# Performance work log

Measured on AMD Instinct MI355X. Metric: run time of the kernel, lower is better.

Reference implementation:

```python
import jax, jax.numpy as jnp
import numpy as np

D_MODEL = 1024
H = 16
D_K = D_MODEL // H


def setup_inputs() -> dict:
    key = jax.random.key(0)
    ks = jax.random.split(key, 8)
    B, S = 2, 2048
    q = jax.random.normal(ks[0], (B, S, D_MODEL), dtype=jnp.float32)
    k = jax.random.normal(ks[1], (B, S, D_MODEL), dtype=jnp.float32)
    v = jax.random.normal(ks[2], (B, S, D_MODEL), dtype=jnp.float32)
    mask = jnp.ones((B, 1, S), dtype=jnp.int32)  # key-padding mask, 1 = keep
    sc = 1.0 / np.sqrt(D_MODEL)
    # torch Linear weights [out, in]
    Wq = jax.random.normal(ks[3], (D_MODEL, D_MODEL), dtype=jnp.float32) * sc
    Wk = jax.random.normal(ks[4], (D_MODEL, D_MODEL), dtype=jnp.float32) * sc
    Wv = jax.random.normal(ks[5], (D_MODEL, D_MODEL), dtype=jnp.float32) * sc
    Wo = jax.random.normal(ks[6], (D_MODEL, D_MODEL), dtype=jnp.float32) * sc
    return {"q": q, "k": k, "v": v, "mask": mask,
            "Wq": Wq, "Wk": Wk, "Wv": Wv, "Wo": Wo}


def reference(q, k, v, mask, Wq, Wk, Wv, Wo):
    B, Sq, _ = q.shape
    Sk = k.shape[1]
    # projections (torch Linear: x @ W.T), split heads -> [B, H, S, d_k]
    def split_heads(x, W, S):
        return (x @ W.T).reshape(B, S, H, D_K).transpose(0, 2, 1, 3)
    qh = split_heads(q, Wq, Sq)
    kh = split_heads(k, Wk, Sk)
    vh = split_heads(v, Wv, Sk)
    scores = jnp.einsum('bhqd,bhkd->bhqk', qh, kh) / jnp.sqrt(
        jnp.asarray(D_K, qh.dtype))
    # mask.unsqueeze(1): [B,1,S] -> [B,1,1,S]; masked_fill(mask==0, -1e9)
    m = mask[:, None, :, :]
    scores = jnp.where(m == 0, jnp.asarray(-1e9, scores.dtype), scores)
    p = jax.nn.softmax(scores, axis=-1)
    out = jnp.einsum('bhqk,bhkd->bhqd', p, vh)
    out = out.transpose(0, 2, 1, 3).reshape(B, Sq, H * D_K)
    return out @ Wo.T
```

## Files before the change

### kernel.cpp

```cpp
#include <hip/hip_runtime.h>
#include <hip/hip_bf16.h>

#define LOG2E 1.4426950408889634f

typedef __attribute__((ext_vector_type(8))) __bf16 bf16x8;
typedef __attribute__((ext_vector_type(2))) __bf16 bf16x2;
typedef __attribute__((ext_vector_type(4))) float f32x4;
typedef __attribute__((ext_vector_type(16))) float f32x16;

#define MFMA16(a,b,c) __builtin_amdgcn_mfma_f32_16x16x32_bf16((a),(b),(c),0,0,0)
#define MFMA32(a,b,c) __builtin_amdgcn_mfma_f32_32x32x16_bf16((a),(b),(c),0,0,0)

#define GLL16(g, l) __builtin_amdgcn_global_load_lds( \
    (const __attribute__((address_space(1))) void*)(g), \
    (__attribute__((address_space(3))) void*)(l), 16, 0, 0)

__device__ __forceinline__ unsigned short bfu(float f) {
    __bf16 h = (__bf16)f; unsigned short u; __builtin_memcpy(&u, &h, 2); return u;
}
__device__ __forceinline__ unsigned cvtpk(float lo, float hi) {
    bf16x2 t; t.x = (__bf16)lo; t.y = (__bf16)hi;
    unsigned r; __builtin_memcpy(&r, &t, 4); return r;
}
__device__ __forceinline__ bf16x8 pack4(unsigned a, unsigned b, unsigned c, unsigned d) {
    union { unsigned u[4]; bf16x8 v; } t; t.u[0]=a; t.u[1]=b; t.u[2]=c; t.u[3]=d; return t.v;
}
__device__ __forceinline__ bf16x8 cvt8(float4 a, float4 b, float s) {
    bf16x8 o;
    o[0]=(__bf16)(a.x*s); o[1]=(__bf16)(a.y*s); o[2]=(__bf16)(a.z*s); o[3]=(__bf16)(a.w*s);
    o[4]=(__bf16)(b.x*s); o[5]=(__bf16)(b.y*s); o[6]=(__bf16)(b.z*s); o[7]=(__bf16)(b.w*s);
    return o;
}

__device__ __forceinline__ size_t kidx(int bh, int s, int d) {
    int kt = s>>6, half=(s>>5)&1, l31k=s&31;
    int dc=d>>4, hik=(d>>3)&1, e=d&7;
    return (((size_t)bh*32+kt)*8 + half*4+dc)*512 + (hik*32+l31k)*8 + e;
}
__device__ __forceinline__ size_t vidx(int bh, int s, int d) {
    int kt=s>>6, kvin=s&63, kc=kvin>>4, rem=kvin&15;
    int hiv=(rem>>2)&1, e=(rem&3)+4*(rem>>3);
    int v1=d>>5, l31v=d&31;
    return (((size_t)bh*32+kt)*8 + kc*2+v1)*512 + (hiv*32+l31v)*8 + e;
}

__global__ __launch_bounds__(256)
void conv_kernel(const float* __restrict__ q, const float* __restrict__ k,
                 const float* __restrict__ v, const float* __restrict__ Wq,
                 const float* __restrict__ Wk, const float* __restrict__ Wv,
                 const float* __restrict__ Wo, unsigned short* __restrict__ Xb,
                 unsigned short* __restrict__ Wb)
{
    const int y = blockIdx.y;
    if (y < 3) {
        const float* s = (y==0)?q:(y==1)?k:v;
        size_t i = ((size_t)blockIdx.x*256 + threadIdx.x)*8;
        float4 a = *(const float4*)(s+i), b = *(const float4*)(s+i+4);
        *(bf16x8*)(Xb + (size_t)y*4194304 + i) = cvt8(a, b, 1.0f);
    } else {
        const int w = blockIdx.x >> 9;
        const float* s = (w==0)?Wq:(w==1)?Wk:(w==2)?Wv:Wo;
        const float sc = (w==0) ? 0.125f*LOG2E : 1.0f;
        size_t i = ((size_t)(blockIdx.x & 511)*256 + threadIdx.x)*8;
        float4 a = *(const float4*)(s+i), b = *(const float4*)(s+i+4);
        *(bf16x8*)(Wb + (size_t)w*1048576 + i) = cvt8(a, b, sc);
    }
}

__global__ __launch_bounds__(256)
void qkv_kernel(const unsigned short* __restrict__ Xb,
                const unsigned short* __restrict__ Wb,
                unsigned short* __restrict__ Qh, unsigned short* __restrict__ Kg,
                unsigned short* __restrict__ Vg)
{
    __shared__ unsigned short As[3][4096];
    __shared__ unsigned short Bs[3][4096];
    const int z = blockIdx.z;
    const unsigned short* X = Xb + (size_t)z*4194304;
    const unsigned short* W = Wb + (size_t)z*1048576;
    const int t = threadIdx.x, wid = t>>6, lane = t&63;
    const int m0 = blockIdx.x*128, n0 = blockIdx.y*128;
    const int wr = (wid>>1)*64, wc = (wid&1)*64;
    const int lr = lane&15, lk = lane>>4;

    f32x4 acc[4][4] = {};

#define STAGEQ(ktile, buf) do { \
    const int K0_ = (ktile)*32; \
    _Pragma("unroll") \
    for (int i_=0;i_<2;++i_){ \
        int flat_ = i_*4096 + wid*1024 + lane*16; \
        int row_ = flat_>>6, cb_ = (flat_&63) ^ ((row_&3)<<4); \
        GLL16(X + (size_t)(m0+row_)*1024 + K0_ + (cb_>>1), (char*)&As[buf][0] + i_*4096 + wid*1024); \
        GLL16(W + (size_t)(n0+row_)*1024 + K0_ + (cb_>>1), (char*)&Bs[buf][0] + i_*4096 + wid*1024); \
    } } while (0)

    STAGEQ(0, 0);

    for (int kt=0; kt<32; ++kt){
        const int cur = kt % 3;
        if (kt < 31) {
            STAGEQ(kt+1, (kt+1)%3);
            asm volatile("s_waitcnt vmcnt(4)" ::: "memory");
        } else {
            asm volatile("s_waitcnt vmcnt(0)" ::: "memory");
        }
        __builtin_amdgcn_s_barrier();
        asm volatile("" ::: "memory");

        bf16x8 a[4], b[4];
#pragma unroll
        for (int i=0;i<4;++i){
            int row = wr+i*16+lr;
            a[i] = *(const bf16x8*)((const char*)&As[cur][0] + row*64 + ((lk*16)^((row&3)<<4)));
        }
#pragma unroll
        for (int j=0;j<4;++j){
            int row = wc+j*16+lr;
            b[j] = *(const bf16x8*)((const char*)&Bs[cur][0] + row*64 + ((lk*16)^((row&3)<<4)));
        }
#pragma unroll
        for (int i=0;i<4;++i)
#pragma unroll
            for (int j=0;j<4;++j)
                acc[i][j] = MFMA16(a[i], b[j], acc[i][j]);
    }
#undef STAGEQ

#pragma unroll
    for (int i=0;i<4;++i)
#pragma unroll
      for (int j=0;j<4;++j)
#pragma unroll
        for (int r=0;r<4;++r){
            int m = m0 + wr + i*16 + lk*4 + r;
            int n = n0 + wc + j*16 + lr;
            int b_ = m>>11, s = m&2047;
            int h = n>>6, d = n&63;
            int bh = b_*16 + h;
            unsigned short val = bfu(acc[i][j][r]);
            if (z==0)      Qh[((size_t)bh*2048 + s)*64 + d] = val;
            else if (z==1) Kg[kidx(bh, s, d)] = val;
            else           Vg[vidx(bh, s, d)] = val;
        }
}

__global__ __launch_bounds__(256)
void oproj_kernel(const unsigned short* __restrict__ Oh,
                  const unsigned short* __restrict__ Wo,
                  float* __restrict__ out)
{
    __shared__ unsigned short As[2][8192];
    __shared__ unsigned short Bs2[2][4096];
    const int t = threadIdx.x, wid = t>>6, lane = t&63;
    const int m0 = blockIdx.x*128, n0 = blockIdx.y*64;
    const int wr = (wid>>1)*64, wc = (wid&1)*32;
    const int lr = lane&15, lk = lane>>4;
    const int fbase = wid*1024 + lane*16;

    f32x4 acc[4][2] = {};

#pragma unroll
    for (int i=0;i<4;++i){
        int flat = i*4096 + fbase, row = flat>>7;
        int cb = (flat&127) ^ ((row&7)<<4);
        int m = m0+row, b_ = m>>11, s = m&2047;
        GLL16(Oh + ((size_t)(b_*16+0)*2048 + s)*64 + (cb>>1), (char*)&As[0][0] + i*4096 + wid*1024);
    }
#pragma unroll
    for (int i=0;i<2;++i){
        int flat = i*4096 + fbase, row = flat>>7;
        int cb = (flat&127) ^ ((row&7)<<4);
        GLL16(Wo + (size_t)(n0+row)*1024 + (cb>>1), (char*)&Bs2[0][0] + i*4096 + wid*1024);
    }

    for (int kt=0; kt<16; ++kt){
        const int cur = kt&1;
        if (kt<15){
            const int nb = cur^1, K0 = (kt+1)*64, h = K0>>6;
#pragma unroll
            for (int i=0;i<4;++i){
                int flat = i*4096 + fbase, row = flat>>7;
                int cb = (flat&127) ^ ((row&7)<<4);
                int m = m0+row, b_ = m>>11, s = m&2047;
                GLL16(Oh + ((size_t)(b_*16+h)*2048 + s)*64 + (cb>>1),
                      (char*)&As[nb][0] + i*4096 + wid*1024);
            }
#pragma unroll
            for (int i=0;i<2;++i){
                int flat = i*4096 + fbase, row = flat>>7;
                int cb = (flat&127) ^ ((row&7)<<4);
                GLL16(Wo + (size_t)(n0+row)*1024 + K0 + (cb>>1),
                      (char*)&Bs2[nb][0] + i*4096 + wid*1024);
            }
            asm volatile("s_waitcnt vmcnt(6)" ::: "memory");
        } else {
            asm volatile("s_waitcnt vmcnt(0)" ::: "memory");
        }
        __builtin_amdgcn_s_barrier();
        asm volatile("" ::: "memory");

        bf16x8 a[4][2], b[2][2];
#pragma unroll
        for (int i=0;i<4;++i){
            int row = wr+i*16+lr, sw = (row&7)<<4;
            const char* rp = (const char*)&As[cur][0] + row*128;
#pragma unroll
            for (int ks=0;ks<2;++ks)
                a[i][ks] = *(const bf16x8*)(rp + ((ks*64 + lk*16)^sw));
        }
#pragma unroll
        for (int j=0;j<2;++j){
            int row = wc+j*16+lr, sw = (row&7)<<4;
            const char* rp = (const char*)&Bs2[cur][0] + row*128;
#pragma unroll
            for (int ks=0;ks<2;++ks)
                b[j][ks] = *(const bf16x8*)(rp + ((ks*64 + lk*16)^sw));
        }
#pragma unroll
        for (int i=0;i<4;++i)
#pragma unroll
          for (int j=0;j<2;++j)
#pragma unroll
            for (int ks=0;ks<2;++ks)
                acc[i][j] = MFMA16(a[i][ks], b[j][ks], acc[i][j]);
        asm volatile("" ::: "memory");
        __builtin_amdgcn_s_barrier();
    }

#pragma unroll
    for (int i=0;i<4;++i)
#pragma unroll
      for (int j=0;j<2;++j)
#pragma unroll
        for (int r=0;r<4;++r){
            int m = m0 + wr + i*16 + lk*4 + r;
            int n = n0 + wc + j*16 + lr;
            out[(size_t)m*1024 + n] = acc[i][j][r];
        }
}

__global__ __launch_bounds__(256, 2)
void attn_kernel(const unsigned short* __restrict__ Qh,
                 const unsigned short* __restrict__ Kg,
                 const unsigned short* __restrict__ Vg,
                 const int* __restrict__ mask,
                 unsigned short* __restrict__ Oh)
{
    __shared__ unsigned short Ks[4][4096];

    const int t = threadIdx.x, wid = t >> 6, lane = t & 63;
    const int l31 = lane & 31, hi = lane >> 5;
    const int linb = blockIdx.x + 16*blockIdx.y;
    const int work = (linb & 7)*64 + (linb >> 3);
    const int bh = work >> 4;
    const int q0 = (work & 15) * 128;
    const int b_ = bh >> 4;
    const int qw = q0 + wid*32 + l31;

    unsigned flagbits;
    {
        const int4* mp = (const int4*)(mask + b_*2048 + (lane&31)*64);
        int bad = 0;
#pragma unroll
        for (int i=0;i<16;++i){ int4 m4 = mp[i];
            bad |= (m4.x==0)|(m4.y==0)|(m4.z==0)|(m4.w==0); }
        unsigned long long bm = __ballot(bad);
        flagbits = (unsigned)bm;
    }

    bf16x8 qf[4];
    const unsigned short* Qp = Qh + ((size_t)bh*2048 + qw)*64 + hi*8;
#pragma unroll
    for (int dc = 0; dc < 4; ++dc) qf[dc] = *(const bf16x8*)(Qp + dc*16);

    const unsigned short* Kbase = Kg + (size_t)bh*131072;
    const unsigned short* Vb2   = Vg + (size_t)bh*131072 + lane*8;

#define STAGE(ktile, buf) do { \
    const unsigned short* Kt_ = Kbase + (size_t)(ktile)*4096; \
    _Pragma("unroll") \
    for (int i_ = 0; i_ < 2; ++i_) { \
        int g_ = wid*2 + i_; \
        GLL16(Kt_ + g_*512 + lane*8, &Ks[buf][g_*512]); \
    } } while (0)

    STAGE(0, 0);
    STAGE(1, 1);

    f32x16 o0a = {}, o0b = {}, o1a = {}, o1b = {};
    float l_run = 0.0f;
    f32x16 minit;
#pragma unroll
    for (int r = 0; r < 16; ++r) minit[r] = -12.0f;

    for (int kt = 0; kt < 32; ++kt) {
        const int cur = kt & 3;
        if (kt < 31) asm volatile("s_waitcnt vmcnt(2)" ::: "memory");
        else         asm volatile("s_waitcnt vmcnt(0)" ::: "memory");
        __builtin_amdgcn_s_barrier();
        asm volatile("" ::: "memory");

        bf16x8 kb[8];
#pragma unroll
        for (int f = 0; f < 8; ++f) kb[f] = *(const bf16x8*)&Ks[cur][f*512 + lane*8];

        bf16x8 vf[8];
        {
            const unsigned short* vp = Vb2 + (size_t)kt*4096;
#pragma unroll
            for (int g = 0; g < 8; ++g) vf[g] = *(const bf16x8*)(vp + g*512);
        }
        asm volatile("" ::: "memory");

        f32x16 s0, s1;
#pragma unroll
        for (int dc = 0; dc < 4; ++dc) {
            if (dc == 0) { s0 = MFMA32(kb[0], qf[0], minit); s1 = MFMA32(kb[4], qf[0], minit); }
            else         { s0 = MFMA32(kb[dc], qf[dc], s0);  s1 = MFMA32(kb[4+dc], qf[dc], s1); }
        }

        if (kt + 2 < 32) STAGE(kt + 2, (kt + 2) & 3);
        asm volatile("" ::: "memory");

        if (flagbits & (1u << kt)) {
            const int* mrow = mask + b_*2048 + kt*64;
#pragma unroll
            for (int r = 0; r < 16; ++r) {
                int kv = (r&3) + 8*(r>>2) + 4*hi;
                if (mrow[kv] == 0)      s0[r] = -1e9f;
                if (mrow[32 + kv] == 0) s1[r] = -1e9f;
            }
        }

#pragma unroll
        for (int r = 0; r < 16; ++r) {
            s0[r] = __builtin_amdgcn_exp2f(s0[r]);
            s1[r] = __builtin_amdgcn_exp2f(s1[r]);
        }

        {
            float rs = 0.0f;
#pragma unroll
            for (int r = 0; r < 16; ++r) rs += s0[r] + s1[r];
            l_run += rs;
        }

        bf16x8 pa[4];
        pa[0] = pack4(cvtpk(s0[0],s0[1]),  cvtpk(s0[2],s0[3]),
                      cvtpk(s0[4],s0[5]),  cvtpk(s0[6],s0[7]));
        pa[1] = pack4(cvtpk(s0[8],s0[9]),  cvtpk(s0[10],s0[11]),
                      cvtpk(s0[12],s0[13]),cvtpk(s0[14],s0[15]));
        pa[2] = pack4(cvtpk(s1[0],s1[1]),  cvtpk(s1[2],s1[3]),
                      cvtpk(s1[4],s1[5]),  cvtpk(s1[6],s1[7]));
        pa[3] = pack4(cvtpk(s1[8],s1[9]),  cvtpk(s1[10],s1[11]),
                      cvtpk(s1[12],s1[13]),cvtpk(s1[14],s1[15]));

        o0a = MFMA32(pa[0], vf[0], o0a);
        o1a = MFMA32(pa[0], vf[1], o1a);
        o0b = MFMA32(pa[1], vf[2], o0b);
        o1b = MFMA32(pa[1], vf[3], o1b);
        o0a = MFMA32(pa[2], vf[4], o0a);
        o1a = MFMA32(pa[2], vf[5], o1a);
        o0b = MFMA32(pa[3], vf[6], o0b);
        o1b = MFMA32(pa[3], vf[7], o1b);
    }
#undef STAGE

    f32x16 o0, o1;
#pragma unroll
    for (int r = 0; r < 16; ++r) { o0[r] = o0a[r] + o0b[r]; o1[r] = o1a[r] + o1b[r]; }
    float l_tot = l_run + __shfl_xor(l_run, 32);

    float cc[16];
    {
        float* Lb = (float*)((char*)&Ks[0][0] + wid*256);
        Lb[l31] = l_tot;
        asm volatile("s_waitcnt lgkmcnt(0)" ::: "memory");
#pragma unroll
        for (int g = 0; g < 4; ++g) {
            float4 v = *(const float4*)&Lb[g*8 + hi*4];
            cc[4*g]=v.x; cc[4*g+1]=v.y; cc[4*g+2]=v.z; cc[4*g+3]=v.w;
        }
    }

    unsigned short* Ob = Oh + ((size_t)bh*2048 + q0 + wid*32)*64;
#pragma unroll
    for (int r = 0; r < 16; ++r) {
        int qr = (r&3) + 8*(r>>2) + 4*hi;
        float inv = 1.0f / cc[r];
        Ob[(size_t)qr*64 + l31]      = bfu(o0[r] * inv);
        Ob[(size_t)qr*64 + 32 + l31] = bfu(o1[r] * inv);
    }
}

extern "C" void kernel_launch(void* const* d_in, const int* in_sizes, int n_in,
                              void* d_out, int out_size, void* d_ws, size_t ws_size,
                              hipStream_t stream)
{
    const float* q  = (const float*)d_in[0];
    const float* k  = (const float*)d_in[1];
    const float* v  = (const float*)d_in[2];
    const int* mask = (const int*)d_in[3];
    const float* Wq = (const float*)d_in[4];
    const float* Wk = (const float*)d_in[5];
    const float* Wv = (const float*)d_in[6];
    const float* Wo = (const float*)d_in[7];
    float* out = (float*)d_out;

    unsigned short* Xb = (unsigned short*)d_ws;
    unsigned short* Wb = Xb + (size_t)12582912;
    unsigned short* Qh = Wb + (size_t)4194304;
    unsigned short* Kg = Qh + (size_t)4194304;
    unsigned short* Vg = Kg + (size_t)4194304;
    unsigned short* Oh = Xb;

    conv_kernel<<<dim3(2048,4), 256, 0, stream>>>(q, k, v, Wq, Wk, Wv, Wo, Xb, Wb);
    qkv_kernel<<<dim3(32,8,3), 256, 0, stream>>>(Xb, Wb, Qh, Kg, Vg);
    attn_kernel<<<dim3(16,32), 256, 0, stream>>>(Qh, Kg, Vg, mask, Oh);
    oproj_kernel<<<dim3(32,16), 256, 0, stream>>>(Oh, Wb + (size_t)3145728, out);
}
```

Measured before the change: 118.7 us.

## Process two key tiles per iteration with an 8-deep LDS prefetch ring

```diff
diff --git a/kernel.cpp b/kernel.cpp
--- a/kernel.cpp
+++ b/kernel.cpp
@@ -247,7 +247,7 @@
                  const int* __restrict__ mask,
                  unsigned short* __restrict__ Oh)
 {
-    __shared__ unsigned short Ks[4][4096];
+    __shared__ unsigned short Ks[8][4096];
 
     const int t = threadIdx.x, wid = t >> 6, lane = t & 63;
     const int l31 = lane & 31, hi = lane >> 5;
@@ -277,16 +277,15 @@
     const unsigned short* Kbase = Kg + (size_t)bh*131072;
     const unsigned short* Vb2   = Vg + (size_t)bh*131072 + lane*8;
 
-#define STAGE(ktile, buf) do { \
+#define STAGE(ktile) do { if ((ktile) < 32) { \
     const unsigned short* Kt_ = Kbase + (size_t)(ktile)*4096; \
     _Pragma("unroll") \
     for (int i_ = 0; i_ < 2; ++i_) { \
         int g_ = wid*2 + i_; \
-        GLL16(Kt_ + g_*512 + lane*8, &Ks[buf][g_*512]); \
-    } } while (0)
-
-    STAGE(0, 0);
-    STAGE(1, 1);
+        GLL16(Kt_ + g_*512 + lane*8, &Ks[(ktile)&7][g_*512]); \
+    } } } while (0)
+
+    STAGE(0); STAGE(1); STAGE(2); STAGE(3);
 
     f32x16 o0a = {}, o0b = {}, o1a = {}, o1b = {};
     float l_run = 0.0f;
@@ -294,58 +293,74 @@
 #pragma unroll
     for (int r = 0; r < 16; ++r) minit[r] = -12.0f;
 
-    for (int kt = 0; kt < 32; ++kt) {
-        const int cur = kt & 3;
-        if (kt < 31) asm volatile("s_waitcnt vmcnt(2)" ::: "memory");
-        else         asm volatile("s_waitcnt vmcnt(0)" ::: "memory");
+    asm volatile("s_waitcnt vmcnt(4)" ::: "memory");
+
+    for (int it = 0; it < 16; ++it) {
+        const int ta = 2*it, tb = 2*it + 1;
         __builtin_amdgcn_s_barrier();
         asm volatile("" ::: "memory");
 
-        bf16x8 kb[8];
-#pragma unroll
-        for (int f = 0; f < 8; ++f) kb[f] = *(const bf16x8*)&Ks[cur][f*512 + lane*8];
-
-        bf16x8 vf[8];
+        bf16x8 vfa[8], vfb[8];
         {
-            const unsigned short* vp = Vb2 + (size_t)kt*4096;
-#pragma unroll
-            for (int g = 0; g < 8; ++g) vf[g] = *(const bf16x8*)(vp + g*512);
-        }
+            const unsigned short* vp = Vb2 + (size_t)ta*4096;
+#pragma unroll
+            for (int g = 0; g < 8; ++g) {
+                vfa[g] = *(const bf16x8*)(vp + g*512);
+                vfb[g] = *(const bf16x8*)(vp + 4096 + g*512);
+            }
+        }
+
+        f32x16 s0, s1;
+        {
+            bf16x8 ka[8];
+#pragma unroll
+            for (int f = 0; f < 8; ++f) ka[f] = *(const bf16x8*)&Ks[ta&7][f*512 + lane*8];
+#pragma unroll
+            for (int dc = 0; dc < 4; ++dc) {
+                if (dc == 0) { s0 = MFMA32(ka[0], qf[0], minit); s1 = MFMA32(ka[4], qf[0], minit); }
+                else         { s0 = MFMA32(ka[dc], qf[dc], s0);  s1 = MFMA32(ka[4+dc], qf[dc], s1); }
+            }
+        }
+
+        STAGE(ta + 4); STAGE(tb + 4);
         asm volatile("" ::: "memory");
 
-        f32x16 s0, s1;
-#pragma unroll
-        for (int dc = 0; dc < 4; ++dc) {
-            if (dc == 0) { s0 = MFMA32(kb[0], qf[0], minit); s1 = MFMA32(kb[4], qf[0], minit); }
-            else         { s0 = MFMA32(kb[dc], qf[dc], s0);  s1 = MFMA32(kb[4+dc], qf[dc], s1); }
-        }
-
-        if (kt + 2 < 32) STAGE(kt + 2, (kt + 2) & 3);
-        asm volatile("" ::: "memory");
-
-        if (flagbits & (1u << kt)) {
-            const int* mrow = mask + b_*2048 + kt*64;
+        f32x16 u0, u1;
+        {
+            bf16x8 kb2[8];
+#pragma unroll
+            for (int f = 0; f < 8; ++f) kb2[f] = *(const bf16x8*)&Ks[tb&7][f*512 + lane*8];
+#pragma unroll
+            for (int dc = 0; dc < 4; ++dc) {
+                if (dc == 0) { u0 = MFMA32(kb2[0], qf[0], minit); u1 = MFMA32(kb2[4], qf[0], minit); }
+                else         { u0 = MFMA32(kb2[dc], qf[dc], u0);  u1 = MFMA32(kb2[4+dc], qf[dc], u1); }
+            }
+        }
+
+        if (flagbits & (3u << ta)) {
+            const int* mrow = mask + b_*2048 + ta*64;
 #pragma unroll
             for (int r = 0; r < 16; ++r) {
                 int kv = (r&3) + 8*(r>>2) + 4*hi;
-                if (mrow[kv] == 0)      s0[r] = -1e9f;
-                if (mrow[32 + kv] == 0) s1[r] = -1e9f;
-            }
-        }
-
+                if (flagbits & (1u << ta)) {
+                    if (mrow[kv] == 0)      s0[r] = -1e9f;
+                    if (mrow[32 + kv] == 0) s1[r] = -1e9f;
+                }
+                if (flagbits & (1u << tb)) {
+                    if (mrow[64 + kv] == 0)  u0[r] = -1e9f;
+                    if (mrow[96 + kv] == 0)  u1[r] = -1e9f;
+                }
+            }
+        }
+
+        float rs = 0.0f;
 #pragma unroll
         for (int r = 0; r < 16; ++r) {
             s0[r] = __builtin_amdgcn_exp2f(s0[r]);
             s1[r] = __builtin_amdgcn_exp2f(s1[r]);
         }
-
-        {
-            float rs = 0.0f;
-#pragma unroll
-            for (int r = 0; r < 16; ++r) rs += s0[r] + s1[r];
-            l_run += rs;
-        }
-
+#pragma unroll
+        for (int r = 0; r < 16; ++r) rs += s0[r] + s1[r];
         bf16x8 pa[4];
         pa[0] = pack4(cvtpk(s0[0],s0[1]),  cvtpk(s0[2],s0[3]),
                       cvtpk(s0[4],s0[5]),  cvtpk(s0[6],s0[7]));
@@ -356,14 +371,42 @@
         pa[3] = pack4(cvtpk(s1[8],s1[9]),  cvtpk(s1[10],s1[11]),
                       cvtpk(s1[12],s1[13]),cvtpk(s1[14],s1[15]));
 
-        o0a = MFMA32(pa[0], vf[0], o0a);
-        o1a = MFMA32(pa[0], vf[1], o1a);
-        o0b = MFMA32(pa[1], vf[2], o0b);
-        o1b = MFMA32(pa[1], vf[3], o1b);
-        o0a = MFMA32(pa[2], vf[4], o0a);
-        o1a = MFMA32(pa[2], vf[5], o1a);
-        o0b = MFMA32(pa[3], vf[6], o0b);
-        o1b = MFMA32(pa[3], vf[7], o1b);
+        o0a = MFMA32(pa[0], vfa[0], o0a);
+        o1a = MFMA32(pa[0], vfa[1], o1a);
+        o0b = MFMA32(pa[1], vfa[2], o0b);
+        o1b = MFMA32(pa[1], vfa[3], o1b);
+        o0a = MFMA32(pa[2], vfa[4], o0a);
+        o1a = MFMA32(pa[2], vfa[5], o1a);
+        o0b = MFMA32(pa[3], vfa[6], o0b);
+        o1b = MFMA32(pa[3], vfa[7], o1b);
+
+#pragma unroll
+        for (int r = 0; r < 16; ++r) {
+            u0[r] = __builtin_amdgcn_exp2f(u0[r]);
+            u1[r] = __builtin_amdgcn_exp2f(u1[r]);
+        }
+#pragma unroll
+        for (int r = 0; r < 16; ++r) rs += u0[r] + u1[r];
+        bf16x8 pb[4];
+        pb[0] = pack4(cvtpk(u0[0],u0[1]),  cvtpk(u0[2],u0[3]),
+                      cvtpk(u0[4],u0[5]),  cvtpk(u0[6],u0[7]));
+        pb[1] = pack4(cvtpk(u0[8],u0[9]),  cvtpk(u0[10],u0[11]),
+                      cvtpk(u0[12],u0[13]),cvtpk(u0[14],u0[15]));
+        pb[2] = pack4(cvtpk(u1[0],u1[1]),  cvtpk(u1[2],u1[3]),
+                      cvtpk(u1[4],u1[5]),  cvtpk(u1[6],u1[7]));
+        pb[3] = pack4(cvtpk(u1[8],u1[9]),  cvtpk(u1[10],u1[11]),
+                      cvtpk(u1[12],u1[13]),cvtpk(u1[14],u1[15]));
+
+        o0a = MFMA32(pb[0], vfb[0], o0a);
+        o1a = MFMA32(pb[0], vfb[1], o1a);
+        o0b = MFMA32(pb[1], vfb[2], o0b);
+        o1b = MFMA32(pb[1], vfb[3], o1b);
+        o0a = MFMA32(pb[2], vfb[4], o0a);
+        o1a = MFMA32(pb[2], vfb[5], o1a);
+        o0b = MFMA32(pb[3], vfb[6], o0b);
+        o1b = MFMA32(pb[3], vfb[7], o1b);
+
+        l_run += rs;
     }
 #undef STAGE
 
```

Result: slower. 121.2 us (+2.1%).

## Split attention KV range across two wave groups and merge partial outputs in LDS

Applied to the files above, without the earlier changes.

```diff
diff --git a/kernel.cpp b/kernel.cpp
--- a/kernel.cpp
+++ b/kernel.cpp
@@ -240,23 +240,24 @@
         }
 }
 
-__global__ __launch_bounds__(256, 2)
+__global__ __launch_bounds__(512, 4)
 void attn_kernel(const unsigned short* __restrict__ Qh,
                  const unsigned short* __restrict__ Kg,
                  const unsigned short* __restrict__ Vg,
                  const int* __restrict__ mask,
                  unsigned short* __restrict__ Oh)
 {
-    __shared__ unsigned short Ks[4][4096];
+    __shared__ unsigned short Ks[8][4096];
 
     const int t = threadIdx.x, wid = t >> 6, lane = t & 63;
+    const int qwid = wid & 3, half = wid >> 2;
     const int l31 = lane & 31, hi = lane >> 5;
     const int linb = blockIdx.x + 16*blockIdx.y;
     const int work = (linb & 7)*64 + (linb >> 3);
     const int bh = work >> 4;
     const int q0 = (work & 15) * 128;
     const int b_ = bh >> 4;
-    const int qw = q0 + wid*32 + l31;
+    const int qw = q0 + qwid*32 + l31;
 
     unsigned flagbits;
     {
@@ -274,19 +275,19 @@
 #pragma unroll
     for (int dc = 0; dc < 4; ++dc) qf[dc] = *(const bf16x8*)(Qp + dc*16);
 
-    const unsigned short* Kbase = Kg + (size_t)bh*131072;
-    const unsigned short* Vb2   = Vg + (size_t)bh*131072 + lane*8;
-
-#define STAGE(ktile, buf) do { \
-    const unsigned short* Kt_ = Kbase + (size_t)(ktile)*4096; \
+    const unsigned short* Kbase = Kg + (size_t)bh*131072 + (size_t)half*65536;
+    const unsigned short* Vb2   = Vg + (size_t)bh*131072 + (size_t)half*65536 + lane*8;
+
+#define STAGE(j) do { if ((j) < 16) { \
+    const unsigned short* Kt_ = Kbase + (size_t)(j)*4096; \
     _Pragma("unroll") \
     for (int i_ = 0; i_ < 2; ++i_) { \
-        int g_ = wid*2 + i_; \
-        GLL16(Kt_ + g_*512 + lane*8, &Ks[buf][g_*512]); \
-    } } while (0)
-
-    STAGE(0, 0);
-    STAGE(1, 1);
+        int g_ = qwid*2 + i_; \
+        GLL16(Kt_ + g_*512 + lane*8, &Ks[half*4 + ((j)&3)][g_*512]); \
+    } } } while (0)
+
+    STAGE(0);
+    STAGE(1);
 
     f32x16 o0a = {}, o0b = {}, o1a = {}, o1b = {};
     float l_run = 0.0f;
@@ -294,20 +295,21 @@
 #pragma unroll
     for (int r = 0; r < 16; ++r) minit[r] = -12.0f;
 
-    for (int kt = 0; kt < 32; ++kt) {
-        const int cur = kt & 3;
-        if (kt < 31) asm volatile("s_waitcnt vmcnt(2)" ::: "memory");
-        else         asm volatile("s_waitcnt vmcnt(0)" ::: "memory");
+    for (int i = 0; i < 16; ++i) {
+        const int kt = half*16 + i;
+        if (i < 15) asm volatile("s_waitcnt vmcnt(2)" ::: "memory");
+        else        asm volatile("s_waitcnt vmcnt(0)" ::: "memory");
         __builtin_amdgcn_s_barrier();
         asm volatile("" ::: "memory");
 
         bf16x8 kb[8];
 #pragma unroll
-        for (int f = 0; f < 8; ++f) kb[f] = *(const bf16x8*)&Ks[cur][f*512 + lane*8];
+        for (int f = 0; f < 8; ++f)
+            kb[f] = *(const bf16x8*)&Ks[half*4 + (i&3)][f*512 + lane*8];
 
         bf16x8 vf[8];
         {
-            const unsigned short* vp = Vb2 + (size_t)kt*4096;
+            const unsigned short* vp = Vb2 + (size_t)i*4096;
 #pragma unroll
             for (int g = 0; g < 8; ++g) vf[g] = *(const bf16x8*)(vp + g*512);
         }
@@ -320,7 +322,7 @@
             else         { s0 = MFMA32(kb[dc], qf[dc], s0);  s1 = MFMA32(kb[4+dc], qf[dc], s1); }
         }
 
-        if (kt + 2 < 32) STAGE(kt + 2, (kt + 2) & 3);
+        STAGE(i + 2);
         asm volatile("" ::: "memory");
 
         if (flagbits & (1u << kt)) {
@@ -372,25 +374,47 @@
     for (int r = 0; r < 16; ++r) { o0[r] = o0a[r] + o0b[r]; o1[r] = o1a[r] + o1b[r]; }
     float l_tot = l_run + __shfl_xor(l_run, 32);
 
-    float cc[16];
-    {
-        float* Lb = (float*)((char*)&Ks[0][0] + wid*256);
-        Lb[l31] = l_tot;
-        asm volatile("s_waitcnt lgkmcnt(0)" ::: "memory");
-#pragma unroll
-        for (int g = 0; g < 4; ++g) {
-            float4 v = *(const float4*)&Lb[g*8 + hi*4];
-            cc[4*g]=v.x; cc[4*g+1]=v.y; cc[4*g+2]=v.z; cc[4*g+3]=v.w;
-        }
-    }
-
-    unsigned short* Ob = Oh + ((size_t)bh*2048 + q0 + wid*32)*64;
-#pragma unroll
-    for (int r = 0; r < 16; ++r) {
-        int qr = (r&3) + 8*(r>>2) + 4*hi;
-        float inv = 1.0f / cc[r];
-        Ob[(size_t)qr*64 + l31]      = bfu(o0[r] * inv);
-        Ob[(size_t)qr*64 + 32 + l31] = bfu(o1[r] * inv);
+    __syncthreads();
+    float* Mf = (float*)&Ks[0][0];
+    if (half == 1) {
+        float* M = Mf + qwid*2112;
+#pragma unroll
+        for (int r = 0; r < 16; ++r) {
+            M[r*64 + lane]      = o0[r];
+            M[(16+r)*64 + lane] = o1[r];
+        }
+        M[2048 + lane] = l_tot;
+    }
+    __syncthreads();
+    if (half == 0) {
+        const float* M = Mf + qwid*2112;
+#pragma unroll
+        for (int r = 0; r < 16; ++r) {
+            o0[r] += M[r*64 + lane];
+            o1[r] += M[(16+r)*64 + lane];
+        }
+        l_tot += M[2048 + lane];
+
+        float cc[16];
+        {
+            float* Lb = Mf + 8448 + qwid*64;
+            Lb[l31] = l_tot;
+            asm volatile("s_waitcnt lgkmcnt(0)" ::: "memory");
+#pragma unroll
+            for (int g = 0; g < 4; ++g) {
+                float4 v = *(const float4*)&Lb[g*8 + hi*4];
+                cc[4*g]=v.x; cc[4*g+1]=v.y; cc[4*g+2]=v.z; cc[4*g+3]=v.w;
+            }
+        }
+
+        unsigned short* Ob = Oh + ((size_t)bh*2048 + q0 + qwid*32)*64;
+#pragma unroll
+        for (int r = 0; r < 16; ++r) {
+            int qr = (r&3) + 8*(r>>2) + 4*hi;
+            float inv = 1.0f / cc[r];
+            Ob[(size_t)qr*64 + l31]      = bfu(o0[r] * inv);
+            Ob[(size_t)qr*64 + 32 + l31] = bfu(o1[r] * inv);
+        }
     }
 }
 
@@ -417,6 +441,6 @@
 
     conv_kernel<<<dim3(2048,4), 256, 0, stream>>>(q, k, v, Wq, Wk, Wv, Wo, Xb, Wb);
     qkv_kernel<<<dim3(32,8,3), 256, 0, stream>>>(Xb, Wb, Qh, Kg, Vg);
-    attn_kernel<<<dim3(16,32), 256, 0, stream>>>(Qh, Kg, Vg, mask, Oh);
+    attn_kernel<<<dim3(16,32), 512, 0, stream>>>(Qh, Kg, Vg, mask, Oh);
     oproj_kernel<<<dim3(32,16), 256, 0, stream>>>(Oh, Wb + (size_t)3145728, out);
 }
```

Measured after the change: 322.3 us. 171% more time.
